# Optimization experiments

Measured on AMD Instinct MI355X. Metric: run time of the kernel, lower is better.

The kernel has to match this reference:

```python
import jax, jax.numpy as jnp
import numpy as np

B, T, UD, YD, ZD, HD, L = 1024, 1024, 16, 16, 16, 128, 2


def setup_inputs() -> dict:
    key = jax.random.key(0)
    ks = iter(jax.random.split(key, 40))
    r = lambda *s: jax.random.normal(next(ks), s, jnp.float32) * 0.05
    inp = dict(
        u=jax.random.normal(next(ks), (B, UD, T), jnp.float32),
        y=jax.random.normal(next(ks), (B, YD, T), jnp.float32),
        h0=jax.random.uniform(next(ks), (L, B, HD), jnp.float32),
        phi_u_w0=r(HD, UD), phi_u_b0=r(HD), phi_u_w1=r(HD, HD), phi_u_b1=r(HD),
        dynn_w0=r(HD, 2 * HD), dynn_b0=r(HD), dynn_w1=r(HD, HD), dynn_b1=r(HD),
        x_mean_w=r(ZD, HD), x_mean_b=r(ZD),
        x_logvar_w=r(ZD, HD), x_logvar_b=r(ZD),
        phi_x_w0=r(HD, 2 * ZD), phi_x_b0=r(HD), phi_x_w1=r(HD, HD), phi_x_b1=r(HD),
        menn_w0=r(HD, HD), menn_b0=r(HD), menn_w1=r(YD, HD), menn_b1=r(YD),
        gru_wih=r(L, 3 * HD, HD), gru_whh=r(L, 3 * HD, HD),
        C=r(YD, ZD),
    )
    return inp


def _mlp2(x, w0, b0, w1, b1):
    # Linear -> ReLU -> Linear (torch Linear: y = x W^T + b)
    return jax.nn.relu(x @ w0.T + b0) @ w1.T + b1


def reference(u, y, h0,
              phi_u_w0, phi_u_b0, phi_u_w1, phi_u_b1,
              dynn_w0, dynn_b0, dynn_w1, dynn_b1,
              x_mean_w, x_mean_b, x_logvar_w, x_logvar_b,
              phi_x_w0, phi_x_b0, phi_x_w1, phi_x_b1,
              menn_w0, menn_b0, menn_w1, menn_b1,
              gru_wih, gru_whh, C):
    uT = jnp.moveaxis(u, 2, 0)  # (T, B, UD)
    yT = jnp.moveaxis(y, 2, 0)  # (T, B, YD)

    def step(h, xy):
        u_t, y_t = xy
        phi_u_t = _mlp2(u_t, phi_u_w0, phi_u_b0, phi_u_w1, phi_u_b1)  # (B, HD)
        dphi = _mlp2(jnp.concatenate([phi_u_t, h[-1]], axis=1),
                     dynn_w0, dynn_b0, dynn_w1, dynn_b1)
        x_mean = dphi @ x_mean_w.T + x_mean_b      # (B, ZD)
        x_logvar = dphi @ x_logvar_w.T + x_logvar_b
        # single-step multi-layer GRU (no bias), PyTorch gate order r,z,n
        x = phi_u_t
        hs = []
        for l in range(L):
            gi = x @ gru_wih[l].T          # (B, 3HD)
            gh = h[l] @ gru_whh[l].T
            ir, iz, inn = jnp.split(gi, 3, axis=1)
            hr, hz, hn = jnp.split(gh, 3, axis=1)
            rg = jax.nn.sigmoid(ir + hr)
            zg = jax.nn.sigmoid(iz + hz)
            ng = jnp.tanh(inn + rg * hn)
            hl = (1.0 - zg) * ng + zg * h[l]
            hs.append(hl)
            x = hl
        h_new = jnp.stack(hs, axis=0)
        # mpnt_wt >= 10 branch: NN measurement + physics measurement C @ x_mean
        phi_x = _mlp2(jnp.concatenate([x_mean, x_logvar], axis=1),
                      phi_x_w0, phi_x_b0, phi_x_w1, phi_x_b1)
        y_hat = _mlp2(phi_x, menn_w0, menn_b0, menn_w1, menn_b1) + x_mean @ C.T
        loss_t = jnp.sum((y_hat - y_t) ** 2)
        return h_new, loss_t

    _, losses = jax.lax.scan(step, h0, (uT, yT))
    return jnp.sum(losses)
```

## Files before the change

kernel.cpp:

```cpp
#include <hip/hip_runtime.h>
#include <hip/hip_bf16.h>

typedef unsigned short u16;
typedef unsigned int u32;
using short8 = __attribute__((ext_vector_type(8))) short;
using f32x4  = __attribute__((ext_vector_type(4))) float;

#define DEVINL static __device__ __forceinline__

DEVINL float bf2f(u16 u){
  union { unsigned int i; float f; } x; x.i = ((unsigned int)u) << 16; return x.f;
}
DEVINL u16 f2bf(float f){
  union { float f; unsigned int i; } x; x.f = f;
  unsigned int i = x.i;
  return (u16)((i + 0x7FFFu + ((i >> 16) & 1u)) >> 16);
}
DEVINL u16 f2bf1(float f){
  __hip_bfloat16 b = __float2bfloat16(f);
  u16 u; __builtin_memcpy(&u, &b, 2); return u;
}
DEVINL float fast_sigm(float x){
  float e = __builtin_amdgcn_exp2f(x * -1.442695041f);
  return __builtin_amdgcn_rcpf(1.f + e);
}
DEVINL float fast_tanh(float x){
  x = fminf(fmaxf(x, -10.f), 10.f);
  float e = __builtin_amdgcn_exp2f(x * -2.885390082f);
  return (1.f - e) * __builtin_amdgcn_rcpf(1.f + e);
}
DEVINL f32x4 zero4(){ f32x4 z = {0.f, 0.f, 0.f, 0.f}; return z; }

DEVINL f32x4 mfma16(short8 a, short8 b, f32x4 c){
  return __builtin_amdgcn_mfma_f32_16x16x32_bf16(a, b, c, 0, 0, 0);
}

DEVINL short8 frag_ld(const u16* base, int stride){
  int l = threadIdx.x & 63;
  return *(const short8*)(base + (l & 15) * stride + ((l >> 4) << 3));
}
DEVINL short8 gfrag(const u16* rowbase, int stride, int ks){
  int l = threadIdx.x & 63;
  return *(const short8*)(rowbase + (size_t)(l & 15) * stride + ks * 32 + ((l >> 4) << 3));
}

DEVINL void acc_store_lds(u16* dst, int stride, int col_base, f32x4 acc, float bias, bool relu){
  int l = threadIdx.x & 63;
  int col = col_base + (l & 15);
  int row0 = (l >> 4) * 4;
  #pragma unroll
  for (int r = 0; r < 4; r++){
    float v = acc[r] + bias;
    if (relu) v = fmaxf(v, 0.f);
    dst[(row0 + r) * stride + col] = f2bf(v);
  }
}

DEVINL void stage_weights(u16* dst, const float* src, int N, int K, int Kp){
  int stride = Kp + 8;
  if (Kp > K){
    int padw = Kp - K;
    for (int i = threadIdx.x; i < N * padw; i += blockDim.x){
      int n = i / padw, k = K + (i - (i / padw) * padw);
      dst[n * stride + k] = 0;
    }
  }
  for (int i = threadIdx.x * 4; i < N * K; i += blockDim.x * 4){
    float4 v = *(const float4*)(src + i);
    int n = i / K, k = i - n * K;
    u16* d = dst + n * stride + k;
    d[0] = f2bf(v.x); d[1] = f2bf(v.y); d[2] = f2bf(v.z); d[3] = f2bf(v.w);
  }
}

__global__ __launch_bounds__(256) void k_inith(const float* __restrict__ h0, u16* __restrict__ hst){
  int i = blockIdx.x * 256 + threadIdx.x;
  if (i < 2 * 1024 * 128) hst[i] = f2bf(h0[i]);
}


DEVINL void phiu_body(u16* smem, int idx, const float* u, const float* w0, const float* b0,
                      const float* w1, const float* b1, u16* phiW, int t0, int Tc){
  u16* w0s = smem;
  u16* w1s = smem + 5120;
  u16* buf = smem + 22528;
  stage_weights(w0s, w0, 128, 16, 32);
  stage_weights(w1s, w1, 128, 128, 128);
  int wv = threadIdx.x >> 6, l = threadIdx.x & 63;
  u16* mybuf = buf + wv * 2176;
  float b0v[8], b1v[8];
  #pragma unroll
  for (int nt = 0; nt < 8; nt++){
    b0v[nt] = b0[nt * 16 + (l & 15)];
    b1v[nt] = b1[nt * 16 + (l & 15)];
  }
  __syncthreads();
  int tpb = Tc >> 4;
  int ntile = 1024 * tpb;
  for (int tile = idx * 4 + wv; tile < ntile; tile += 112 * 4){
    int b = tile / tpb;
    int tt = (tile - b * tpb) << 4;
    int t = l & 15, kb = l >> 4;
    #pragma unroll
    for (int j = 0; j < 4; j++){
      int k = kb + j * 4;
      mybuf[t * 136 + k] = f2bf(u[(size_t)(b * 16 + k) * 1024 + t0 + tt + t]);
      mybuf[t * 136 + 16 + k] = 0;
    }
    short8 a0 = frag_ld(mybuf, 136);
    f32x4 acc[8];
    #pragma unroll
    for (int nt = 0; nt < 8; nt++)
      acc[nt] = mfma16(a0, frag_ld(w0s + nt * 16 * 40, 40), zero4());
    #pragma unroll
    for (int nt = 0; nt < 8; nt++)
      acc_store_lds(mybuf, 136, nt * 16, acc[nt], b0v[nt], true);
    f32x4 a2[8];
    #pragma unroll
    for (int nt = 0; nt < 8; nt++) a2[nt] = zero4();
    #pragma unroll
    for (int ks = 0; ks < 4; ks++){
      short8 a = frag_ld(mybuf + ks * 32, 136);
      #pragma unroll
      for (int nt = 0; nt < 8; nt++)
        a2[nt] = mfma16(a, frag_ld(w1s + nt * 16 * 136 + ks * 32, 136), a2[nt]);
    }
    #pragma unroll
    for (int nt = 0; nt < 8; nt++)
      acc_store_lds(mybuf, 136, nt * 16, a2[nt], b1v[nt], false);
    u16* dst = phiW + (size_t)(b * Tc + tt) * 128;
    #pragma unroll
    for (int j = 0; j < 4; j++){
      int c = j * 64 + l;
      int row = c >> 4, k = (c & 15) * 8;
      *(short8*)(dst + row * 128 + k) = *(const short8*)(mybuf + row * 136 + k);
    }
  }
}

DEVINL void gru_body(u16* smem, int idx, const u16* __restrict__ phi,
                     const float* gwih, const float* gwhh,
                     u16* hst, u16* Hs, int Tc){
  u16* wi0 = smem;
  u16* h0sA[2] = { smem + 52224, smem + 54400 };
  u16* h1sA[2] = { smem + 56576, smem + 58752 };
  u16* pbA[4]  = { smem + 60928, smem + 63104, smem + 65280, smem + 67456 };
  const int l = threadIdx.x & 63;
  const int wv = threadIdx.x >> 6;
  const int b0 = idx * 16;
  const int m0 = (l >> 4) * 4;
  const int cc = l & 15;
  const int nb = wv * 32;

  stage_weights(wi0, gwih, 384, 128, 128);

  const float* srcs[3] = { gwhh, gwih + 49152, gwhh + 49152 };
  short8 Wr[3][3][2][4];
  #pragma unroll
  for (int mm = 0; mm < 3; mm++){
    #pragma unroll
    for (int g = 0; g < 3; g++){
      #pragma unroll
      for (int nt = 0; nt < 2; nt++){
        int n = g * 128 + nb + nt * 16 + cc;
        #pragma unroll
        for (int ks = 0; ks < 4; ks++){
          const float* p = srcs[mm] + (size_t)n * 128 + ks * 32 + ((l >> 4) << 3);
          float4 va = *(const float4*)p;
          float4 vb = *(const float4*)(p + 4);
          short8 f;
          f[0] = (short)f2bf(va.x); f[1] = (short)f2bf(va.y);
          f[2] = (short)f2bf(va.z); f[3] = (short)f2bf(va.w);
          f[4] = (short)f2bf(vb.x); f[5] = (short)f2bf(vb.y);
          f[6] = (short)f2bf(vb.z); f[7] = (short)f2bf(vb.w);
          Wr[mm][g][nt][ks] = f;
        }
      }
    }
  }
  const int row = threadIdx.x >> 4, k0 = (threadIdx.x & 15) * 8;
  *(uint4*)(&h0sA[0][row * 136 + k0]) = *(const uint4*)(hst + (size_t)(b0 + row) * 128 + k0);
  *(uint4*)(&h1sA[0][row * 136 + k0]) = *(const uint4*)(hst + 131072 + (size_t)(b0 + row) * 128 + k0);
  float hp0[2][4], hp1[2][4];
  #pragma unroll
  for (int nt = 0; nt < 2; nt++)
    #pragma unroll
    for (int r = 0; r < 4; r++){
      hp0[nt][r] = bf2f(hst[(size_t)(b0 + m0 + r) * 128 + nb + nt * 16 + cc]);
      hp1[nt][r] = bf2f(hst[131072 + (size_t)(b0 + m0 + r) * 128 + nb + nt * 16 + cc]);
    }
  const u16* pL = phi + (size_t)(b0 + row) * Tc * 128 + k0;
  u16* Hp = Hs + (size_t)(b0 + row) * Tc * 128 + k0;
  *(uint4*)(&pbA[0][row * 136 + k0]) = *(const uint4*)(pL);
  *(uint4*)(&pbA[1][row * 136 + k0]) = *(const uint4*)(pL + 128);
  uint4 pfA = *(const uint4*)(pL + 2 * 128);
  uint4 pfB = *(const uint4*)(pL + 3 * 128);
  __syncthreads();

  auto ITER = [&](int i, int P, int q, uint4& pf){
    short8 a0[4];
    #pragma unroll
    for (int ks = 0; ks < 4; ks++) a0[ks] = frag_ld(h0sA[P] + ks * 32, 136);
    if (i > 0){
      short8 a1[4];
      #pragma unroll
      for (int ks = 0; ks < 4; ks++) a1[ks] = frag_ld(h1sA[P ^ 1] + ks * 32, 136);
      *(uint4*)(Hp + (size_t)(i - 1) * 128) = *(const uint4*)(&h1sA[P ^ 1][row * 136 + k0]);
      f32x4 cr[2], cz[2], cin[2], chn[2];
      #pragma unroll
      for (int nt = 0; nt < 2; nt++){ cr[nt]=zero4(); cz[nt]=zero4(); cin[nt]=zero4(); chn[nt]=zero4(); }
      #pragma unroll
      for (int ks = 0; ks < 4; ks++)
        #pragma unroll
        for (int nt = 0; nt < 2; nt++){
          cr[nt]  = mfma16(a0[ks], Wr[1][0][nt][ks], cr[nt]);
          cr[nt]  = mfma16(a1[ks], Wr[2][0][nt][ks], cr[nt]);
          cz[nt]  = mfma16(a0[ks], Wr[1][1][nt][ks], cz[nt]);
          cz[nt]  = mfma16(a1[ks], Wr[2][1][nt][ks], cz[nt]);
          cin[nt] = mfma16(a0[ks], Wr[1][2][nt][ks], cin[nt]);
          chn[nt] = mfma16(a1[ks], Wr[2][2][nt][ks], chn[nt]);
        }
      #pragma unroll
      for (int nt = 0; nt < 2; nt++)
        #pragma unroll
        for (int r = 0; r < 4; r++){
          float rg = fast_sigm(cr[nt][r]);
          float zg = fast_sigm(cz[nt][r]);
          float ng = fast_tanh(cin[nt][r] + rg * chn[nt][r]);
          float hv = zg * (hp1[nt][r] - ng) + ng;
          hp1[nt][r] = hv;
          h1sA[P][(m0 + r) * 136 + nb + nt * 16 + cc] = f2bf1(hv);
        }
    }
    if (i < Tc){
      short8 ap[4];
      #pragma unroll
      for (int ks = 0; ks < 4; ks++) ap[ks] = frag_ld(pbA[q] + ks * 32, 136);
      f32x4 cr[2], cz[2], cin[2], chn[2];
      #pragma unroll
      for (int nt = 0; nt < 2; nt++){ cr[nt]=zero4(); cz[nt]=zero4(); cin[nt]=zero4(); chn[nt]=zero4(); }
      #pragma unroll
      for (int ks = 0; ks < 4; ks++)
        #pragma unroll
        for (int nt = 0; nt < 2; nt++){
          cr[nt]  = mfma16(ap[ks], frag_ld(wi0 + (0 * 128 + nb + nt * 16) * 136 + ks * 32, 136), cr[nt]);
          cr[nt]  = mfma16(a0[ks], Wr[0][0][nt][ks], cr[nt]);
          cz[nt]  = mfma16(ap[ks], frag_ld(wi0 + (1 * 128 + nb + nt * 16) * 136 + ks * 32, 136), cz[nt]);
          cz[nt]  = mfma16(a0[ks], Wr[0][1][nt][ks], cz[nt]);
          cin[nt] = mfma16(ap[ks], frag_ld(wi0 + (2 * 128 + nb + nt * 16) * 136 + ks * 32, 136), cin[nt]);
          chn[nt] = mfma16(a0[ks], Wr[0][2][nt][ks], chn[nt]);
        }
      if (i + 2 < Tc) *(uint4*)(&pbA[(q + 2) & 3][row * 136 + k0]) = pf;
      if (i + 4 < Tc) pf = *(const uint4*)(pL + (size_t)(i + 4) * 128);
      #pragma unroll
      for (int nt = 0; nt < 2; nt++)
        #pragma unroll
        for (int r = 0; r < 4; r++){
          float rg = fast_sigm(cr[nt][r]);
          float zg = fast_sigm(cz[nt][r]);
          float ng = fast_tanh(cin[nt][r] + rg * chn[nt][r]);
          float hv = zg * (hp0[nt][r] - ng) + ng;
          hp0[nt][r] = hv;
          h0sA[P ^ 1][(m0 + r) * 136 + nb + nt * 16 + cc] = f2bf1(hv);
        }
    }
    __builtin_amdgcn_sched_barrier(0);
    asm volatile("s_waitcnt lgkmcnt(0)");
    __builtin_amdgcn_s_barrier();
    __builtin_amdgcn_sched_barrier(0);
  };

  for (int i = 0; i < Tc; i += 4){
    ITER(i + 0, 0, 0, pfA);
    ITER(i + 1, 1, 1, pfB);
    ITER(i + 2, 0, 2, pfA);
    ITER(i + 3, 1, 3, pfB);
  }
  ITER(Tc, 0, 0, pfA);
  *(uint4*)(hst + (size_t)(b0 + row) * 128 + k0) = *(const uint4*)(&h0sA[0][row * 136 + k0]);
  *(uint4*)(hst + 131072 + (size_t)(b0 + row) * 128 + k0) = *(const uint4*)(&h1sA[0][row * 136 + k0]);
}

DEVINL void c1_body(u16* smem, int idx, const u16* phiC, const u16* HsC,
    const float* dw0, const float* db0, const float* dw1, const float* db1,
    const float* xmw, const float* xmb, const float* xlw, const float* xlb,
    u16* xmlv, int Tc){
  u16* w0s = smem;
  u16* w1s = smem + 33792;
  u16* xws = smem + 51200;
  u16* buf = smem + 55552;
  stage_weights(w0s, dw0, 128, 256, 256);
  stage_weights(w1s, dw1, 128, 128, 128);
  stage_weights(xws, xmw, 16, 128, 128);
  stage_weights(xws + 16 * 136, xlw, 16, 128, 128);
  int wv = threadIdx.x >> 6, l = threadIdx.x & 63;
  u16* mybuf = buf + wv * 2176;
  float b0v[8], b1v[8];
  #pragma unroll
  for (int nt = 0; nt < 8; nt++){
    b0v[nt] = db0[nt * 16 + (l & 15)];
    b1v[nt] = db1[nt * 16 + (l & 15)];
  }
  float bxm = xmb[l & 15], bxl = xlb[l & 15];
  __syncthreads();
  int tpb = Tc >> 4;
  int ntile = 1024 * tpb;
  for (int tile = idx * 4 + wv; tile < ntile; tile += 112 * 4){
    int b = tile / tpb;
    int tt = (tile - b * tpb) << 4;
    size_t rbase = (size_t)(b * Tc + tt);
    const u16* ap = phiC + rbase * 128;
    const u16* hp = HsC + rbase * 128;
    f32x4 acc[8];
    #pragma unroll
    for (int nt = 0; nt < 8; nt++) acc[nt] = zero4();
    #pragma unroll
    for (int ks = 0; ks < 8; ks++){
      short8 a = (ks < 4) ? gfrag(ap, 128, ks) : gfrag(hp, 128, ks - 4);
      #pragma unroll
      for (int nt = 0; nt < 8; nt++)
        acc[nt] = mfma16(a, frag_ld(w0s + nt * 16 * 264 + ks * 32, 264), acc[nt]);
    }
    #pragma unroll
    for (int nt = 0; nt < 8; nt++)
      acc_store_lds(mybuf, 136, nt * 16, acc[nt], b0v[nt], true);
    f32x4 a2[8];
    #pragma unroll
    for (int nt = 0; nt < 8; nt++) a2[nt] = zero4();
    #pragma unroll
    for (int ks = 0; ks < 4; ks++){
      short8 a = frag_ld(mybuf + ks * 32, 136);
      #pragma unroll
      for (int nt = 0; nt < 8; nt++)
        a2[nt] = mfma16(a, frag_ld(w1s + nt * 16 * 136 + ks * 32, 136), a2[nt]);
    }
    #pragma unroll
    for (int nt = 0; nt < 8; nt++)
      acc_store_lds(mybuf, 136, nt * 16, a2[nt], b1v[nt], false);
    f32x4 am = zero4(), al = zero4();
    #pragma unroll
    for (int ks = 0; ks < 4; ks++){
      short8 a = frag_ld(mybuf + ks * 32, 136);
      am = mfma16(a, frag_ld(xws + ks * 32, 136), am);
      al = mfma16(a, frag_ld(xws + 16 * 136 + ks * 32, 136), al);
    }
    acc_store_lds(mybuf, 136, 0, am, bxm, false);
    acc_store_lds(mybuf, 136, 16, al, bxl, false);
    u16* dst = xmlv + rbase * 32;
    int c = l;
    int row = c >> 2, k = (c & 3) * 8;
    *(short8*)(dst + row * 32 + k) = *(const short8*)(mybuf + row * 136 + k);
  }
}

DEVINL void c2_body(u16* smem, int idx, const u16* xmlv, const float* y,
    const float* pw0, const float* pb0, const float* pw1, const float* pb1,
    const float* mw0, const float* mb0, const float* mw1, const float* mb1,
    const float* Cw, float* out, int t0, int Tc){
  u16* pw0s = smem;
  u16* pw1s = smem + 5120;
  u16* mw0s = smem + 22528;
  u16* mw1s = smem + 39936;
  u16* Cs   = smem + 42112;
  u16* buf  = smem + 42752;
  stage_weights(pw0s, pw0, 128, 32, 32);
  stage_weights(pw1s, pw1, 128, 128, 128);
  stage_weights(mw0s, mw0, 128, 128, 128);
  stage_weights(mw1s, mw1, 16, 128, 128);
  stage_weights(Cs, Cw, 16, 16, 32);
  int wv = threadIdx.x >> 6, l = threadIdx.x & 63;
  u16* mybuf = buf + wv * 2176;
  float bp0v[8], bp1v[8], bm0v[8];
  #pragma unroll
  for (int nt = 0; nt < 8; nt++){
    bp0v[nt] = pb0[nt * 16 + (l & 15)];
    bp1v[nt] = pb1[nt * 16 + (l & 15)];
    bm0v[nt] = mb0[nt * 16 + (l & 15)];
  }
  float bm1 = mb1[l & 15];
  __syncthreads();
  float lacc = 0.f;
  int tpb = Tc >> 4;
  int ntile = 1024 * tpb;
  for (int tile = idx * 4 + wv; tile < ntile; tile += 112 * 4){
    int b = tile / tpb;
    int tt = (tile - b * tpb) << 4;
    size_t rbase = (size_t)(b * Tc + tt);
    const u16* xp = xmlv + rbase * 32;
    short8 a0 = gfrag(xp, 32, 0);
    f32x4 acc[8];
    #pragma unroll
    for (int nt = 0; nt < 8; nt++)
      acc[nt] = mfma16(a0, frag_ld(pw0s + nt * 16 * 40, 40), zero4());
    #pragma unroll
    for (int nt = 0; nt < 8; nt++)
      acc_store_lds(mybuf, 136, nt * 16, acc[nt], bp0v[nt], true);
    f32x4 a2[8];
    #pragma unroll
    for (int nt = 0; nt < 8; nt++) a2[nt] = zero4();
    #pragma unroll
    for (int ks = 0; ks < 4; ks++){
      short8 a = frag_ld(mybuf + ks * 32, 136);
      #pragma unroll
      for (int nt = 0; nt < 8; nt++)
        a2[nt] = mfma16(a, frag_ld(pw1s + nt * 16 * 136 + ks * 32, 136), a2[nt]);
    }
    #pragma unroll
    for (int nt = 0; nt < 8; nt++)
      acc_store_lds(mybuf, 136, nt * 16, a2[nt], bp1v[nt], false);
    f32x4 a3[8];
    #pragma unroll
    for (int nt = 0; nt < 8; nt++) a3[nt] = zero4();
    #pragma unroll
    for (int ks = 0; ks < 4; ks++){
      short8 a = frag_ld(mybuf + ks * 32, 136);
      #pragma unroll
      for (int nt = 0; nt < 8; nt++)
        a3[nt] = mfma16(a, frag_ld(mw0s + nt * 16 * 136 + ks * 32, 136), a3[nt]);
    }
    #pragma unroll
    for (int nt = 0; nt < 8; nt++)
      acc_store_lds(mybuf, 136, nt * 16, a3[nt], bm0v[nt], true);
    f32x4 ay = zero4();
    #pragma unroll
    for (int ks = 0; ks < 4; ks++){
      short8 a = frag_ld(mybuf + ks * 32, 136);
      ay = mfma16(a, frag_ld(mw1s + ks * 32, 136), ay);
    }
    f32x4 ac = mfma16(a0, frag_ld(Cs, 40), zero4());
    #pragma unroll
    for (int r = 0; r < 4; r++){
      float yh = ay[r] + bm1 + ac[r];
      int m = (l >> 4) * 4 + r, j = l & 15;
      float d = yh - y[(size_t)(b * 16 + j) * 1024 + t0 + tt + m];
      lacc += d * d;
    }
  }
  #pragma unroll
  for (int off = 32; off > 0; off >>= 1)
    lacc += __shfl_down(lacc, off);
  if (l == 0) atomicAdd(out, lacc);
}

__global__ __launch_bounds__(256, 1) void k_fused(
    const float* __restrict__ u, const float* __restrict__ y,
    const float* puw0, const float* pub0, const float* puw1, const float* pub1,
    const float* dw0, const float* db0, const float* dw1, const float* db1,
    const float* xmw, const float* xmb, const float* xlw, const float* xlb,
    const float* pxw0, const float* pxb0, const float* pxw1, const float* pxb1,
    const float* mw0, const float* mb0, const float* mw1, const float* mb1,
    const float* Cw, const float* gwih, const float* gwhh,
    u16* phiW, const u16* phiG, const u16* phiC,
    u16* hst, u16* HsW, const u16* HsC,
    u16* xmW, const u16* xmC,
    float* out, int t0phiu, int t0c2, int Tc, int flags){
  __shared__ __align__(16) u16 smem[69632];
  int bi = blockIdx.x;
  int lane8 = bi & 7;
  if (lane8 < 2){
    int gidx = (bi >> 3) * 2 + lane8;
    if (gidx < 64 && (flags & 2))
      gru_body(smem, gidx, phiG, gwih, gwhh, hst, HsW, Tc);
    return;
  }
  int w = (bi >> 3) * 6 + (lane8 - 2);
  int role = w / 112, idx = w - role * 112;
  if (role == 0){
    if (flags & 1) phiu_body(smem, idx, u, puw0, pub0, puw1, pub1, phiW, t0phiu, Tc);
  } else if (role == 1){
    if (flags & 4) c1_body(smem, idx, phiC, HsC, dw0, db0, dw1, db1, xmw, xmb, xlw, xlb, xmW, Tc);
  } else {
    if (flags & 8) c2_body(smem, idx, xmC, y, pxw0, pxb0, pxw1, pxb1, mw0, mb0, mw1, mb1, Cw, out, t0c2, Tc);
  }
}

extern "C" void kernel_launch(void* const* d_in, const int* in_sizes, int n_in,
                              void* d_out, int out_size, void* d_ws, size_t ws_size,
                              hipStream_t stream){
  const float* u    = (const float*)d_in[0];
  const float* y    = (const float*)d_in[1];
  const float* h0   = (const float*)d_in[2];
  const float* puw0 = (const float*)d_in[3];
  const float* pub0 = (const float*)d_in[4];
  const float* puw1 = (const float*)d_in[5];
  const float* pub1 = (const float*)d_in[6];
  const float* dw0  = (const float*)d_in[7];
  const float* db0  = (const float*)d_in[8];
  const float* dw1  = (const float*)d_in[9];
  const float* db1  = (const float*)d_in[10];
  const float* xmw  = (const float*)d_in[11];
  const float* xmb  = (const float*)d_in[12];
  const float* xlw  = (const float*)d_in[13];
  const float* xlb  = (const float*)d_in[14];
  const float* pxw0 = (const float*)d_in[15];
  const float* pxb0 = (const float*)d_in[16];
  const float* pxw1 = (const float*)d_in[17];
  const float* pxb1 = (const float*)d_in[18];
  const float* mw0  = (const float*)d_in[19];
  const float* mb0  = (const float*)d_in[20];
  const float* mw1  = (const float*)d_in[21];
  const float* mb1  = (const float*)d_in[22];
  const float* gwih = (const float*)d_in[23];
  const float* gwhh = (const float*)d_in[24];
  const float* Cw   = (const float*)d_in[25];

  const size_t hstE = (size_t)2 * 1024 * 128;
  int Tc = 128;
  while (Tc > 16){
    size_t needB = (hstE + (size_t)1024 * Tc * (3 * 128 + 2 * 128 + 2 * 32)) * 2 + 4096;
    if (needB <= ws_size) break;
    Tc >>= 1;
  }
  int NC = 1024 / Tc;
  size_t phiSz = (size_t)1024 * Tc * 128;
  size_t xmSz  = (size_t)1024 * Tc * 32;

  u16* hst  = (u16*)d_ws;
  u16* phiB = hst + hstE;
  u16* HsB  = phiB + 3 * phiSz;
  u16* xmB  = HsB + 2 * phiSz;

  hipMemsetAsync(d_out, 0, sizeof(float), stream);
  k_inith<<<1024, 256, 0, stream>>>(h0, hst);

  for (int j = 0; j <= NC + 2; j++){
    int flags = 0;
    if (j < NC) flags |= 1;
    if (j >= 1 && j <= NC) flags |= 2;
    if (j >= 2 && j <= NC + 1) flags |= 4;
    if (j >= 3) flags |= 8;
    int s0 = j % 3, s1 = (j + 2) % 3, s2 = (j + 1) % 3;
    int hw = (j + 1) & 1, hc = j & 1;
    int xw = j & 1, xc = (j + 1) & 1;
    k_fused<<<448, 256, 0, stream>>>(
        u, y,
        puw0, pub0, puw1, pub1,
        dw0, db0, dw1, db1, xmw, xmb, xlw, xlb,
        pxw0, pxb0, pxw1, pxb1, mw0, mb0, mw1, mb1,
        Cw, gwih, gwhh,
        phiB + (size_t)s0 * phiSz, phiB + (size_t)s1 * phiSz, phiB + (size_t)s2 * phiSz,
        hst, HsB + (size_t)hw * phiSz, HsB + (size_t)hc * phiSz,
        xmB + (size_t)xw * xmSz, xmB + (size_t)xc * xmSz,
        (float*)d_out, j * Tc, (j - 3) * Tc, Tc, flags);
  }
}
```

Measured before the change: 3.358 ms.

## Widen fused blocks to 512 threads and keep all GRU weights in registers

The fused pipeline kernel now launches 512-thread blocks. In the GRU role each of 8 waves owns a 16-column slice of all four weight matrices in registers, including the layer-0 input weights that previously came from LDS. Because GRU blocks only occupy the first 64 slots when active, the remaining blocks are split evenly across the phi_u, c1 and c2 roles with a computed role size. This spreads the serial recurrence over more waves and drops LDS weight reads per step, at the cost of more per-wave register pressure and narrower per-thread staging loads.

Measured after the change: 2.764 ms. -17.7%, faster.

```diff
diff --git a/kernel.cpp b/kernel.cpp
--- a/kernel.cpp
+++ b/kernel.cpp
@@ -79,7 +79,7 @@
 }
 
 
-DEVINL void phiu_body(u16* smem, int idx, const float* u, const float* w0, const float* b0,
+DEVINL void phiu_body(u16* smem, int idx, int rs, const float* u, const float* w0, const float* b0,
                       const float* w1, const float* b1, u16* phiW, int t0, int Tc){
   u16* w0s = smem;
   u16* w1s = smem + 5120;
@@ -97,7 +97,7 @@
   __syncthreads();
   int tpb = Tc >> 4;
   int ntile = 1024 * tpb;
-  for (int tile = idx * 4 + wv; tile < ntile; tile += 112 * 4){
+  for (int tile = idx * 8 + wv; tile < ntile; tile += rs * 8){
     int b = tile / tpb;
     int tt = (tile - b * tpb) << 4;
     int t = l & 15, kb = l >> 4;
@@ -141,63 +141,54 @@
 DEVINL void gru_body(u16* smem, int idx, const u16* __restrict__ phi,
                      const float* gwih, const float* gwhh,
                      u16* hst, u16* Hs, int Tc){
-  u16* wi0 = smem;
-  u16* h0sA[2] = { smem + 52224, smem + 54400 };
-  u16* h1sA[2] = { smem + 56576, smem + 58752 };
-  u16* pbA[4]  = { smem + 60928, smem + 63104, smem + 65280, smem + 67456 };
+  u16* h0sA[2] = { smem,        smem + 2176 };
+  u16* h1sA[2] = { smem + 4352, smem + 6528 };
+  u16* pbA[4]  = { smem + 8704, smem + 10880, smem + 13056, smem + 15232 };
   const int l = threadIdx.x & 63;
   const int wv = threadIdx.x >> 6;
   const int b0 = idx * 16;
   const int m0 = (l >> 4) * 4;
-  const int cc = l & 15;
-  const int nb = wv * 32;
-
-  stage_weights(wi0, gwih, 384, 128, 128);
-
-  const float* srcs[3] = { gwhh, gwih + 49152, gwhh + 49152 };
-  short8 Wr[3][3][2][4];
-  #pragma unroll
-  for (int mm = 0; mm < 3; mm++){
+  const int colw = wv * 16 + (l & 15);
+
+  const float* srcs[4] = { gwih, gwhh, gwih + 49152, gwhh + 49152 };
+  short8 W[4][3][4];
+  #pragma unroll
+  for (int mm = 0; mm < 4; mm++){
     #pragma unroll
     for (int g = 0; g < 3; g++){
-      #pragma unroll
-      for (int nt = 0; nt < 2; nt++){
-        int n = g * 128 + nb + nt * 16 + cc;
-        #pragma unroll
-        for (int ks = 0; ks < 4; ks++){
-          const float* p = srcs[mm] + (size_t)n * 128 + ks * 32 + ((l >> 4) << 3);
-          float4 va = *(const float4*)p;
-          float4 vb = *(const float4*)(p + 4);
-          short8 f;
-          f[0] = (short)f2bf(va.x); f[1] = (short)f2bf(va.y);
-          f[2] = (short)f2bf(va.z); f[3] = (short)f2bf(va.w);
-          f[4] = (short)f2bf(vb.x); f[5] = (short)f2bf(vb.y);
-          f[6] = (short)f2bf(vb.z); f[7] = (short)f2bf(vb.w);
-          Wr[mm][g][nt][ks] = f;
-        }
+      int n = g * 128 + colw;
+      #pragma unroll
+      for (int ks = 0; ks < 4; ks++){
+        const float* p = srcs[mm] + (size_t)n * 128 + ks * 32 + ((l >> 4) << 3);
+        float4 va = *(const float4*)p;
+        float4 vb = *(const float4*)(p + 4);
+        short8 f;
+        f[0] = (short)f2bf(va.x); f[1] = (short)f2bf(va.y);
+        f[2] = (short)f2bf(va.z); f[3] = (short)f2bf(va.w);
+        f[4] = (short)f2bf(vb.x); f[5] = (short)f2bf(vb.y);
+        f[6] = (short)f2bf(vb.z); f[7] = (short)f2bf(vb.w);
+        W[mm][g][ks] = f;
       }
     }
   }
-  const int row = threadIdx.x >> 4, k0 = (threadIdx.x & 15) * 8;
-  *(uint4*)(&h0sA[0][row * 136 + k0]) = *(const uint4*)(hst + (size_t)(b0 + row) * 128 + k0);
-  *(uint4*)(&h1sA[0][row * 136 + k0]) = *(const uint4*)(hst + 131072 + (size_t)(b0 + row) * 128 + k0);
-  float hp0[2][4], hp1[2][4];
-  #pragma unroll
-  for (int nt = 0; nt < 2; nt++)
-    #pragma unroll
-    for (int r = 0; r < 4; r++){
-      hp0[nt][r] = bf2f(hst[(size_t)(b0 + m0 + r) * 128 + nb + nt * 16 + cc]);
-      hp1[nt][r] = bf2f(hst[131072 + (size_t)(b0 + m0 + r) * 128 + nb + nt * 16 + cc]);
-    }
+  const int row = threadIdx.x >> 5, k0 = (threadIdx.x & 31) * 4;
+  *(uint2*)(&h0sA[0][row * 136 + k0]) = *(const uint2*)(hst + (size_t)(b0 + row) * 128 + k0);
+  *(uint2*)(&h1sA[0][row * 136 + k0]) = *(const uint2*)(hst + 131072 + (size_t)(b0 + row) * 128 + k0);
+  float hp0[4], hp1[4];
+  #pragma unroll
+  for (int r = 0; r < 4; r++){
+    hp0[r] = bf2f(hst[(size_t)(b0 + m0 + r) * 128 + colw]);
+    hp1[r] = bf2f(hst[131072 + (size_t)(b0 + m0 + r) * 128 + colw]);
+  }
   const u16* pL = phi + (size_t)(b0 + row) * Tc * 128 + k0;
   u16* Hp = Hs + (size_t)(b0 + row) * Tc * 128 + k0;
-  *(uint4*)(&pbA[0][row * 136 + k0]) = *(const uint4*)(pL);
-  *(uint4*)(&pbA[1][row * 136 + k0]) = *(const uint4*)(pL + 128);
-  uint4 pfA = *(const uint4*)(pL + 2 * 128);
-  uint4 pfB = *(const uint4*)(pL + 3 * 128);
+  *(uint2*)(&pbA[0][row * 136 + k0]) = *(const uint2*)(pL);
+  *(uint2*)(&pbA[1][row * 136 + k0]) = *(const uint2*)(pL + 128);
+  uint2 pfA = *(const uint2*)(pL + 2 * 128);
+  uint2 pfB = *(const uint2*)(pL + 3 * 128);
   __syncthreads();
 
-  auto ITER = [&](int i, int P, int q, uint4& pf){
+  auto ITER = [&](int i, int P, int q, uint2& pf){
     short8 a0[4];
     #pragma unroll
     for (int ks = 0; ks < 4; ks++) a0[ks] = frag_ld(h0sA[P] + ks * 32, 136);
@@ -205,64 +196,54 @@
       short8 a1[4];
       #pragma unroll
       for (int ks = 0; ks < 4; ks++) a1[ks] = frag_ld(h1sA[P ^ 1] + ks * 32, 136);
-      *(uint4*)(Hp + (size_t)(i - 1) * 128) = *(const uint4*)(&h1sA[P ^ 1][row * 136 + k0]);
-      f32x4 cr[2], cz[2], cin[2], chn[2];
-      #pragma unroll
-      for (int nt = 0; nt < 2; nt++){ cr[nt]=zero4(); cz[nt]=zero4(); cin[nt]=zero4(); chn[nt]=zero4(); }
-      #pragma unroll
-      for (int ks = 0; ks < 4; ks++)
-        #pragma unroll
-        for (int nt = 0; nt < 2; nt++){
-          cr[nt]  = mfma16(a0[ks], Wr[1][0][nt][ks], cr[nt]);
-          cr[nt]  = mfma16(a1[ks], Wr[2][0][nt][ks], cr[nt]);
-          cz[nt]  = mfma16(a0[ks], Wr[1][1][nt][ks], cz[nt]);
-          cz[nt]  = mfma16(a1[ks], Wr[2][1][nt][ks], cz[nt]);
-          cin[nt] = mfma16(a0[ks], Wr[1][2][nt][ks], cin[nt]);
-          chn[nt] = mfma16(a1[ks], Wr[2][2][nt][ks], chn[nt]);
-        }
-      #pragma unroll
-      for (int nt = 0; nt < 2; nt++)
-        #pragma unroll
-        for (int r = 0; r < 4; r++){
-          float rg = fast_sigm(cr[nt][r]);
-          float zg = fast_sigm(cz[nt][r]);
-          float ng = fast_tanh(cin[nt][r] + rg * chn[nt][r]);
-          float hv = zg * (hp1[nt][r] - ng) + ng;
-          hp1[nt][r] = hv;
-          h1sA[P][(m0 + r) * 136 + nb + nt * 16 + cc] = f2bf1(hv);
-        }
+      *(uint2*)(Hp + (size_t)(i - 1) * 128) = *(const uint2*)(&h1sA[P ^ 1][row * 136 + k0]);
+      f32x4 xr = zero4(), xz = zero4(), xn = zero4();
+      f32x4 hr = zero4(), hz = zero4(), hh = zero4();
+      #pragma unroll
+      for (int ks = 0; ks < 4; ks++){
+        xr = mfma16(a0[ks], W[2][0][ks], xr);
+        xz = mfma16(a0[ks], W[2][1][ks], xz);
+        xn = mfma16(a0[ks], W[2][2][ks], xn);
+        hr = mfma16(a1[ks], W[3][0][ks], hr);
+        hz = mfma16(a1[ks], W[3][1][ks], hz);
+        hh = mfma16(a1[ks], W[3][2][ks], hh);
+      }
+      #pragma unroll
+      for (int r = 0; r < 4; r++){
+        float rg = fast_sigm(xr[r] + hr[r]);
+        float zg = fast_sigm(xz[r] + hz[r]);
+        float ng = fast_tanh(xn[r] + rg * hh[r]);
+        float hv = zg * (hp1[r] - ng) + ng;
+        hp1[r] = hv;
+        h1sA[P][(m0 + r) * 136 + colw] = f2bf1(hv);
+      }
     }
     if (i < Tc){
       short8 ap[4];
       #pragma unroll
       for (int ks = 0; ks < 4; ks++) ap[ks] = frag_ld(pbA[q] + ks * 32, 136);
-      f32x4 cr[2], cz[2], cin[2], chn[2];
-      #pragma unroll
-      for (int nt = 0; nt < 2; nt++){ cr[nt]=zero4(); cz[nt]=zero4(); cin[nt]=zero4(); chn[nt]=zero4(); }
-      #pragma unroll
-      for (int ks = 0; ks < 4; ks++)
-        #pragma unroll
-        for (int nt = 0; nt < 2; nt++){
-          cr[nt]  = mfma16(ap[ks], frag_ld(wi0 + (0 * 128 + nb + nt * 16) * 136 + ks * 32, 136), cr[nt]);
-          cr[nt]  = mfma16(a0[ks], Wr[0][0][nt][ks], cr[nt]);
-          cz[nt]  = mfma16(ap[ks], frag_ld(wi0 + (1 * 128 + nb + nt * 16) * 136 + ks * 32, 136), cz[nt]);
-          cz[nt]  = mfma16(a0[ks], Wr[0][1][nt][ks], cz[nt]);
-          cin[nt] = mfma16(ap[ks], frag_ld(wi0 + (2 * 128 + nb + nt * 16) * 136 + ks * 32, 136), cin[nt]);
-          chn[nt] = mfma16(a0[ks], Wr[0][2][nt][ks], chn[nt]);
-        }
-      if (i + 2 < Tc) *(uint4*)(&pbA[(q + 2) & 3][row * 136 + k0]) = pf;
-      if (i + 4 < Tc) pf = *(const uint4*)(pL + (size_t)(i + 4) * 128);
-      #pragma unroll
-      for (int nt = 0; nt < 2; nt++)
-        #pragma unroll
-        for (int r = 0; r < 4; r++){
-          float rg = fast_sigm(cr[nt][r]);
-          float zg = fast_sigm(cz[nt][r]);
-          float ng = fast_tanh(cin[nt][r] + rg * chn[nt][r]);
-          float hv = zg * (hp0[nt][r] - ng) + ng;
-          hp0[nt][r] = hv;
-          h0sA[P ^ 1][(m0 + r) * 136 + nb + nt * 16 + cc] = f2bf1(hv);
-        }
+      f32x4 xr = zero4(), xz = zero4(), xn = zero4();
+      f32x4 hr = zero4(), hz = zero4(), hh = zero4();
+      #pragma unroll
+      for (int ks = 0; ks < 4; ks++){
+        xr = mfma16(ap[ks], W[0][0][ks], xr);
+        xz = mfma16(ap[ks], W[0][1][ks], xz);
+        xn = mfma16(ap[ks], W[0][2][ks], xn);
+        hr = mfma16(a0[ks], W[1][0][ks], hr);
+        hz = mfma16(a0[ks], W[1][1][ks], hz);
+        hh = mfma16(a0[ks], W[1][2][ks], hh);
+      }
+      if (i + 2 < Tc) *(uint2*)(&pbA[(q + 2) & 3][row * 136 + k0]) = pf;
+      if (i + 4 < Tc) pf = *(const uint2*)(pL + (size_t)(i + 4) * 128);
+      #pragma unroll
+      for (int r = 0; r < 4; r++){
+        float rg = fast_sigm(xr[r] + hr[r]);
+        float zg = fast_sigm(xz[r] + hz[r]);
+        float ng = fast_tanh(xn[r] + rg * hh[r]);
+        float hv = zg * (hp0[r] - ng) + ng;
+        hp0[r] = hv;
+        h0sA[P ^ 1][(m0 + r) * 136 + colw] = f2bf1(hv);
+      }
     }
     __builtin_amdgcn_sched_barrier(0);
     asm volatile("s_waitcnt lgkmcnt(0)");
@@ -277,11 +258,11 @@
     ITER(i + 3, 1, 3, pfB);
   }
   ITER(Tc, 0, 0, pfA);
-  *(uint4*)(hst + (size_t)(b0 + row) * 128 + k0) = *(const uint4*)(&h0sA[0][row * 136 + k0]);
-  *(uint4*)(hst + 131072 + (size_t)(b0 + row) * 128 + k0) = *(const uint4*)(&h1sA[0][row * 136 + k0]);
-}
-
-DEVINL void c1_body(u16* smem, int idx, const u16* phiC, const u16* HsC,
+  *(uint2*)(hst + (size_t)(b0 + row) * 128 + k0) = *(const uint2*)(&h0sA[0][row * 136 + k0]);
+  *(uint2*)(hst + 131072 + (size_t)(b0 + row) * 128 + k0) = *(const uint2*)(&h1sA[0][row * 136 + k0]);
+}
+
+DEVINL void c1_body(u16* smem, int idx, int rs, const u16* phiC, const u16* HsC,
     const float* dw0, const float* db0, const float* dw1, const float* db1,
     const float* xmw, const float* xmb, const float* xlw, const float* xlb,
     u16* xmlv, int Tc){
@@ -305,7 +286,7 @@
   __syncthreads();
   int tpb = Tc >> 4;
   int ntile = 1024 * tpb;
-  for (int tile = idx * 4 + wv; tile < ntile; tile += 112 * 4){
+  for (int tile = idx * 8 + wv; tile < ntile; tile += rs * 8){
     int b = tile / tpb;
     int tt = (tile - b * tpb) << 4;
     size_t rbase = (size_t)(b * Tc + tt);
@@ -353,7 +334,7 @@
   }
 }
 
-DEVINL void c2_body(u16* smem, int idx, const u16* xmlv, const float* y,
+DEVINL void c2_body(u16* smem, int idx, int rs, const u16* xmlv, const float* y,
     const float* pw0, const float* pb0, const float* pw1, const float* pb1,
     const float* mw0, const float* mb0, const float* mw1, const float* mb1,
     const float* Cw, float* out, int t0, int Tc){
@@ -382,7 +363,7 @@
   float lacc = 0.f;
   int tpb = Tc >> 4;
   int ntile = 1024 * tpb;
-  for (int tile = idx * 4 + wv; tile < ntile; tile += 112 * 4){
+  for (int tile = idx * 8 + wv; tile < ntile; tile += rs * 8){
     int b = tile / tpb;
     int tt = (tile - b * tpb) << 4;
     size_t rbase = (size_t)(b * Tc + tt);
@@ -442,7 +423,7 @@
   if (l == 0) atomicAdd(out, lacc);
 }
 
-__global__ __launch_bounds__(256, 1) void k_fused(
+__global__ __launch_bounds__(512, 1) void k_fused(
     const float* __restrict__ u, const float* __restrict__ y,
     const float* puw0, const float* pub0, const float* puw1, const float* pub1,
     const float* dw0, const float* db0, const float* dw1, const float* db1,
@@ -454,23 +435,25 @@
     u16* hst, u16* HsW, const u16* HsC,
     u16* xmW, const u16* xmC,
     float* out, int t0phiu, int t0c2, int Tc, int flags){
-  __shared__ __align__(16) u16 smem[69632];
+  __shared__ __align__(16) u16 smem[72960];
   int bi = blockIdx.x;
-  int lane8 = bi & 7;
-  if (lane8 < 2){
-    int gidx = (bi >> 3) * 2 + lane8;
-    if (gidx < 64 && (flags & 2))
-      gru_body(smem, gidx, phiG, gwih, gwhh, hst, HsW, Tc);
+  bool gruOn = (flags & 2) != 0;
+  if (gruOn && bi < 64){
+    gru_body(smem, bi, phiG, gwih, gwhh, hst, HsW, Tc);
     return;
   }
-  int w = (bi >> 3) * 6 + (lane8 - 2);
-  int role = w / 112, idx = w - role * 112;
+  int wb = gruOn ? 64 : 0;
+  int w = bi - wb;
+  int rs = (448 - wb) / 3;
+  int role = w / rs;
+  int idx = w - role * rs;
+  if (role > 2) return;
   if (role == 0){
-    if (flags & 1) phiu_body(smem, idx, u, puw0, pub0, puw1, pub1, phiW, t0phiu, Tc);
+    if (flags & 1) phiu_body(smem, idx, rs, u, puw0, pub0, puw1, pub1, phiW, t0phiu, Tc);
   } else if (role == 1){
-    if (flags & 4) c1_body(smem, idx, phiC, HsC, dw0, db0, dw1, db1, xmw, xmb, xlw, xlb, xmW, Tc);
+    if (flags & 4) c1_body(smem, idx, rs, phiC, HsC, dw0, db0, dw1, db1, xmw, xmb, xlw, xlb, xmW, Tc);
   } else {
-    if (flags & 8) c2_body(smem, idx, xmC, y, pxw0, pxb0, pxw1, pxb1, mw0, mb0, mw1, mb1, Cw, out, t0c2, Tc);
+    if (flags & 8) c2_body(smem, idx, rs, xmC, y, pxw0, pxb0, pxw1, pxb1, mw0, mb0, mw1, mb1, Cw, out, t0c2, Tc);
   }
 }
 
@@ -532,7 +515,7 @@
     int s0 = j % 3, s1 = (j + 2) % 3, s2 = (j + 1) % 3;
     int hw = (j + 1) & 1, hc = j & 1;
     int xw = j & 1, xc = (j + 1) & 1;
-    k_fused<<<448, 256, 0, stream>>>(
+    k_fused<<<448, 512, 0, stream>>>(
         u, y,
         puw0, pub0, puw1, pub1,
         dw0, db0, dw1, db1, xmw, xmb, xlw, xlb,
```
